# Kernel tuning notes

Measured on AMD Instinct MI355X. Metric: run time of the kernel, lower is better.

The kernel has to match this reference:

```python
import jax, jax.numpy as jnp
import numpy as np

LRELU_SLOPE = 0.2
ACT_GAIN = float(np.sqrt(2.0))  # def_gain of lrelu in StyleGAN2
CLAMP = 256.0


def _affine(w, W, b):
    # StyleGAN2 FullyConnectedLayer: runtime weight gain 1/sqrt(in_features)
    return w @ W.T * (1.0 / np.sqrt(W.shape[1])) + b[None, :]


def _gather(x, fn, pad):
    # zero rows for padding faces appended at the end, then neighborhood gather
    padded = jnp.concatenate([x, jnp.zeros((pad, x.shape[1]), x.dtype)], axis=0)
    return padded[fn]  # [N, K, C]


def _mod_texture_conv(g, styles, wc, wsd, wcr):
    # g: [N, 9, I] gathered neighborhoods; styles: [B, I]
    B, I = styles.shape
    N = g.shape[0]
    F = N // B
    # position-typed 1x1 weights: [self, 4 sides, 4 corners] -> [O, I, 9]
    W = jnp.concatenate([wc[:, :, None],
                         jnp.repeat(wsd[:, :, None], 4, axis=2),
                         jnp.repeat(wcr[:, :, None], 4, axis=2)], axis=2)
    wmod = W[None] * styles[:, None, :, None]                    # [B,O,I,9] modulate
    d = jax.lax.rsqrt(jnp.sum(wmod * wmod, axis=(2, 3)) + 1e-8)  # [B,O] demodulate
    wmod = wmod * d[:, :, None, None]
    out = jnp.einsum('bfki,boik->bfok', g.reshape(B, F, 9, I), wmod)
    return out.max(axis=3).reshape(N, -1)  # MaxPool2d((1,9)) aggregation


def _smooth_upsample(x, pool_map, fn, pad):
    # replicate coarse face features to fine faces, then smooth over 9-neighborhood
    return _gather(x[pool_map], fn, pad).mean(axis=1)


def _act(x, bias):
    # clamp_gain(lrelu(x+b), act_gain*gain, 256*gain) with gain=1
    return jnp.clip(jax.nn.leaky_relu(x + bias[None, :], LRELU_SLOPE) * ACT_GAIN, -CLAMP, CLAMP)


def setup_inputs() -> dict:
    key = jax.random.key(0)
    ks = iter(jax.random.split(key, 40))
    B, Fc, Ff = 1, 32768, 131072
    IN, OUT, GEO, COL, WD = 128, 128, 32, 3, 512
    OC1 = OUT - GEO  # 96
    PAD0, PAD1 = 1024, 4096
    nk = lambda *s: jax.random.normal(next(ks), s, jnp.float32)
    ri = lambda shape, hi: jax.random.randint(next(ks), shape, 0, hi, jnp.int32).astype(jnp.int64)
    return dict(
        x=nk(B * Fc, IN - GEO), shape_feat=nk(B * Fc, GEO), img=nk(B * Fc, COL),
        ws=nk(B, 3, WD),
        fn0=ri((B * Fc, 9), B * Fc + PAD0), fn1=ri((B * Ff, 9), B * Ff + PAD1),
        pool_map0=ri((B * Ff,), B * Fc),
        pad0=PAD0, pad1=PAD1,
        affine0_w=nk(IN, WD), affine0_b=jnp.ones((IN,), jnp.float32),
        w_center0=nk(OUT, IN), w_side0=nk(OUT, IN), w_corner0=nk(OUT, IN),
        noise_strength0=nk(1) * 0.1, bias0=nk(OUT) * 0.1, noise_const0=nk(Ff),
        affine1_w=nk(OUT, WD), affine1_b=jnp.ones((OUT,), jnp.float32),
        w_center1=nk(OC1, OUT), w_side1=nk(OC1, OUT), w_corner1=nk(OC1, OUT),
        noise_strength1=nk(1) * 0.1, bias1=nk(OC1) * 0.1, noise_const1=nk(Ff),
        affine2_w=nk(OC1, WD), affine2_b=jnp.ones((OC1,), jnp.float32),
        w_rgb=nk(COL, OC1), bias_rgb=nk(COL) * 0.1,
    )


def reference(x, shape_feat, img, ws, fn0, fn1, pool_map0, pad0, pad1,
              affine0_w, affine0_b, w_center0, w_side0, w_corner0,
              noise_strength0, bias0, noise_const0,
              affine1_w, affine1_b, w_center1, w_side1, w_corner1,
              noise_strength1, bias1, noise_const1,
              affine2_w, affine2_b, w_rgb, bias_rgb):
    B = ws.shape[0]
    h = jnp.concatenate([x, shape_feat], axis=1)  # [B*Fc, IN]
    # ---- conv0: coarse-level modulated face conv, then SmoothUpsample to fine ----
    s0 = _affine(ws[:, 0], affine0_w, affine0_b)
    h = _mod_texture_conv(_gather(h, fn0, pad0), s0, w_center0, w_side0, w_corner0)
    h = _smooth_upsample(h, pool_map0, fn1, pad1)  # [B*Ff, OUT]
    h = h + jnp.tile(noise_const0[None, :], (B, 1)).reshape(-1, 1) * noise_strength0
    h = _act(h, bias0)
    # ---- conv1: fine-level modulated face conv ----
    s1 = _affine(ws[:, 1], affine1_w, affine1_b)
    h = _mod_texture_conv(_gather(h, fn1, pad1), s1, w_center1, w_side1, w_corner1)
    h = h + jnp.tile(noise_const1[None, :], (B, 1)).reshape(-1, 1) * noise_strength1
    h = _act(h, bias1)  # [B*Ff, 96]
    # ---- torgb: 1x1 modulated conv (demodulate=False), weight_gain on styles ----
    s2 = _affine(ws[:, 2], affine2_w, affine2_b) * (1.0 / np.sqrt(w_rgb.shape[1]))
    xg = _gather(h, fn1[:, :1], pad1)[:, 0]  # kernel_size^2 == 1 -> self gather
    y = jnp.einsum('bfi,oi,bi->bfo', xg.reshape(B, -1, xg.shape[1]), w_rgb, s2)
    y = jnp.clip(y.reshape(xg.shape[0], -1) + bias_rgb[None, :], -CLAMP, CLAMP)
    img_out = _smooth_upsample(img, pool_map0, fn1, pad1) + y
    return h, img_out
```

## Files before the change

### kernel.cpp

```cpp
#include <hip/hip_runtime.h>

#define FC 32768
#define FF 131072
#define LRELU_SLOPE 0.2f
#define ACT_GAIN 1.4142135623730951f
#define CLAMP_V 256.0f

typedef __bf16 bf16x8 __attribute__((ext_vector_type(8)));
typedef float f32x4 __attribute__((ext_vector_type(4)));
typedef float f32x2 __attribute__((ext_vector_type(2)));
typedef unsigned u32x4 __attribute__((ext_vector_type(4)));
typedef unsigned u32x2 __attribute__((ext_vector_type(2)));
typedef unsigned short u16x4 __attribute__((ext_vector_type(4)));

static __device__ __forceinline__ unsigned short f2bf(float f) {
    unsigned u = __float_as_uint(f);
    u += 0x7FFFu + ((u >> 16) & 1u);
    return (unsigned short)(u >> 16);
}
static __device__ __forceinline__ unsigned packbf(float a, float b) {
    return (unsigned)f2bf(a) | ((unsigned)f2bf(b) << 16);
}
static __device__ __forceinline__ float bf2f(unsigned short u) {
    return __uint_as_float(((unsigned)u) << 16);
}
static __device__ __forceinline__ float actf(float v) {
    v = (v < 0.f) ? v * LRELU_SLOPE : v;
    v *= ACT_GAIN;
    return fminf(fmaxf(v, -CLAMP_V), CLAMP_V);
}

__global__ void k_prep2(const float* __restrict__ wsvec,
                        const float* __restrict__ a0w, const float* __restrict__ a0b,
                        const float* __restrict__ a1w, const float* __restrict__ a1b,
                        const float* __restrict__ a2w, const float* __restrict__ a2b,
                        float* __restrict__ s0, float* __restrict__ s1, float* __restrict__ s2,
                        unsigned* __restrict__ zrow)
{
    int lane = threadIdx.x & 63;
    int t = blockIdx.x * 4 + (threadIdx.x >> 6);
    if (t >= 352) {
        if (t == 352) zrow[lane] = 0u;
        return;
    }
    int level, o;
    const float *W, *bptr; float* out;
    if (t < 128)       { level = 0; o = t;       W = a0w; bptr = a0b; out = s0; }
    else if (t < 256)  { level = 1; o = t - 128; W = a1w; bptr = a1b; out = s1; }
    else               { level = 2; o = t - 256; W = a2w; bptr = a2b; out = s2; }
    const float* wrow = wsvec + level * 512;
    const float* Wr = W + (size_t)o * 512;
    f32x4 wa = *(const f32x4*)(wrow + lane * 8);
    f32x4 wb = *(const f32x4*)(wrow + lane * 8 + 4);
    f32x4 va = *(const f32x4*)(Wr + lane * 8);
    f32x4 vb = *(const f32x4*)(Wr + lane * 8 + 4);
    float acc = wa.x * va.x + wa.y * va.y + wa.z * va.z + wa.w * va.w
              + wb.x * vb.x + wb.y * vb.y + wb.z * vb.z + wb.w * vb.w;
    #pragma unroll
    for (int off = 32; off; off >>= 1) acc += __shfl_down(acc, off, 64);
    if (lane == 0) {
        float v = acc * 0.04419417382415922f + bptr[o];
        if (level == 2) v *= 0.10206207261596577f;
        out[o] = v;
    }
}

__global__ void k_misc(const float* __restrict__ x, const float* __restrict__ sf,
                       u16x4* __restrict__ xcat,
                       const int* __restrict__ fn1, const int* __restrict__ pmap,
                       int* __restrict__ cidx)
{
    int b = blockIdx.x;
    if (b < FC * 32 / 256) {
        int gid = b * 256 + threadIdx.x;
        int f = gid >> 5;
        int c4 = (gid & 31) * 4;
        f32x4 v;
        if (c4 < 96) v = *(const f32x4*)(x + (size_t)f * 96 + c4);
        else         v = *(const f32x4*)(sf + (size_t)f * 32 + (c4 - 96));
        u16x4 o;
        o.x = f2bf(v.x); o.y = f2bf(v.y); o.z = f2bf(v.z); o.w = f2bf(v.w);
        xcat[gid] = o;
    } else {
        int gid = (b - FC * 32 / 256) * 256 + threadIdx.x;
        int g = fn1[gid];
        cidx[gid] = ((unsigned)g < FF) ? pmap[g] : -1;
    }
}

__global__ void k_wmod(const float* __restrict__ wc0, const float* __restrict__ wsd0,
                       const float* __restrict__ wcr0, const float* __restrict__ s0,
                       unsigned short* __restrict__ wm0,
                       const float* __restrict__ wc1, const float* __restrict__ wsd1,
                       const float* __restrict__ wcr1, const float* __restrict__ s1,
                       unsigned short* __restrict__ wm1,
                       const float* __restrict__ wrgb, const float* __restrict__ s2,
                       float* __restrict__ wrgbmod)
{
    int b = blockIdx.x;
    int i = threadIdx.x;
    if (b == 224) {
        for (int t = i; t < 288; t += 128) {
            int c = t / 96, k = t % 96;
            wrgbmod[c * 96 + k] = wrgb[c * 96 + k] * s2[k];
        }
        return;
    }
    const float *wc, *wsd, *wcr, *s; unsigned short* out; int o, O;
    if (b < 128) { wc = wc0; wsd = wsd0; wcr = wcr0; s = s0; out = wm0; o = b; O = 128; }
    else         { wc = wc1; wsd = wsd1; wcr = wcr1; s = s1; out = wm1; o = b - 128; O = 96; }
    float sv = s[i];
    float pc = wc[o * 128 + i] * sv;
    float ps = wsd[o * 128 + i] * sv;
    float pr = wcr[o * 128 + i] * sv;
    float part = pc * pc + 4.f * ps * ps + 4.f * pr * pr;
    __shared__ float red[2];
    #pragma unroll
    for (int off = 32; off; off >>= 1) part += __shfl_down(part, off, 64);
    if ((threadIdx.x & 63) == 0) red[threadIdx.x >> 6] = part;
    __syncthreads();
    float d = rsqrtf(red[0] + red[1] + 1e-8f);
    out[(0 * O + o) * 128 + i] = f2bf(pc * d);
    out[(1 * O + o) * 128 + i] = f2bf(ps * d);
    out[(2 * O + o) * 128 + i] = f2bf(pr * d);
}

__launch_bounds__(256, 3)
__global__ void k_gemm0(const unsigned short* __restrict__ xcat, const unsigned short* __restrict__ wm,
                        unsigned* __restrict__ y0)
{
    int lane = threadIdx.x & 63;
    int w = threadIdx.x >> 6;
    int bx = blockIdx.x;
    int t = bx % 3, chunk = bx / 3;
    int fbase = (chunk * 4 + w) * 32;
    int quad = lane >> 4, l15 = lane & 15;
    const char* hb = (const char*)xcat;
    const char* wb = (const char*)wm;

    bf16x8 bfr[2][4];
    #pragma unroll
    for (int nt = 0; nt < 2; ++nt)
        #pragma unroll
        for (int s = 0; s < 4; ++s)
            bfr[nt][s] = *(const bf16x8*)(hb + (size_t)(fbase + nt * 16 + l15) * 256 + s * 64 + quad * 16);

    f32x4 acc[2][8];
    #pragma unroll
    for (int nt = 0; nt < 2; ++nt)
        #pragma unroll
        for (int mt = 0; mt < 8; ++mt)
            #pragma unroll
            for (int r = 0; r < 4; ++r) acc[nt][mt][r] = 0.f;

    #pragma unroll
    for (int s = 0; s < 4; ++s) {
        bf16x8 afr[8];
        #pragma unroll
        for (int mt = 0; mt < 8; ++mt)
            afr[mt] = *(const bf16x8*)(wb + (size_t)(((t * 128 + mt * 16 + l15) * 128 + s * 32 + quad * 8) * 2));
        #pragma unroll
        for (int nt = 0; nt < 2; ++nt)
            #pragma unroll
            for (int mt = 0; mt < 8; ++mt)
                acc[nt][mt] = __builtin_amdgcn_mfma_f32_16x16x32_bf16(afr[mt], bfr[nt][s], acc[nt][mt], 0, 0, 0);
    }

    unsigned* yt = y0 + (size_t)t * FC * 64;
    #pragma unroll
    for (int nt = 0; nt < 2; ++nt) {
        int face = fbase + nt * 16 + l15;
        #pragma unroll
        for (int mt = 0; mt < 8; ++mt) {
            u32x2 v;
            v.x = packbf(acc[nt][mt][0], acc[nt][mt][1]);
            v.y = packbf(acc[nt][mt][2], acc[nt][mt][3]);
            *(u32x2*)(yt + (size_t)face * 64 + mt * 8 + quad * 2) = v;
        }
    }
}

__global__ void k_gather0(const unsigned* __restrict__ y0, const int* __restrict__ fn0,
                          const unsigned* __restrict__ zrow, unsigned* __restrict__ hc0)
{
    int gid = blockIdx.x * 256 + threadIdx.x;
    int g = gid >> 4;
    int c = gid & 15;
    int id[9];
    #pragma unroll
    for (int j = 0; j < 9; ++j) id[j] = fn0[g * 9 + j];
    u32x4 v[9];
    #pragma unroll
    for (int j = 0; j < 9; ++j) {
        int t = (j == 0) ? 0 : (j < 5 ? 1 : 2);
        const unsigned* p = ((unsigned)id[j] < FC) ? (y0 + (size_t)t * FC * 64 + (size_t)id[j] * 64) : zrow;
        v[j] = *(const u32x4*)(p + c * 4);
    }
    u32x4 out;
    #pragma unroll
    for (int k = 0; k < 4; ++k) {
        float m0 = bf2f((unsigned short)v[0][k]);
        float m1 = bf2f((unsigned short)(v[0][k] >> 16));
        #pragma unroll
        for (int j = 1; j < 9; ++j) {
            m0 = fmaxf(m0, bf2f((unsigned short)v[j][k]));
            m1 = fmaxf(m1, bf2f((unsigned short)(v[j][k] >> 16)));
        }
        out[k] = packbf(m0, m1);
    }
    *(u32x4*)(hc0 + (size_t)g * 64 + c * 4) = out;
}

__global__ void k_upsample(const unsigned* __restrict__ hc, const int* __restrict__ cidx,
                           const float* __restrict__ nco0,
                           const float* __restrict__ ns0p, const float* __restrict__ bias0,
                           unsigned* __restrict__ h1u, const unsigned* __restrict__ zrow)
{
    int gid = blockIdx.x * 256 + threadIdx.x;
    int f = gid >> 4;
    int c = gid & 15;
    int id[9];
    #pragma unroll
    for (int j = 0; j < 9; ++j) id[j] = cidx[f * 9 + j];
    u32x4 v[9];
    #pragma unroll
    for (int j = 0; j < 9; ++j) {
        const unsigned* p = (id[j] >= 0) ? (hc + (size_t)id[j] * 64) : zrow;
        v[j] = *(const u32x4*)(p + c * 4);
    }
    float nz = nco0[f] * ns0p[0];
    f32x4 b0 = *(const f32x4*)(bias0 + c * 8);
    f32x4 b1 = *(const f32x4*)(bias0 + c * 8 + 4);
    const float inv9 = 1.f / 9.f;
    u32x4 out;
    #pragma unroll
    for (int k = 0; k < 4; ++k) {
        float a0 = 0.f, a1 = 0.f;
        #pragma unroll
        for (int j = 0; j < 9; ++j) {
            a0 += bf2f((unsigned short)v[j][k]);
            a1 += bf2f((unsigned short)(v[j][k] >> 16));
        }
        float bb0 = (k < 2) ? ((k == 0) ? b0.x : b0.z) : ((k == 2) ? b1.x : b1.z);
        float bb1 = (k < 2) ? ((k == 0) ? b0.y : b0.w) : ((k == 2) ? b1.y : b1.w);
        a0 = actf(a0 * inv9 + nz + bb0);
        a1 = actf(a1 * inv9 + nz + bb1);
        out[k] = packbf(a0, a1);
    }
    *(u32x4*)(h1u + (size_t)f * 64 + c * 4) = out;
}

__launch_bounds__(256, 4)
__global__ void k_gemm1(const unsigned short* __restrict__ h1, const unsigned short* __restrict__ wm,
                        unsigned* __restrict__ ybase)
{
    int lane = threadIdx.x & 63;
    int w = threadIdx.x >> 6;
    int bx = blockIdx.x;
    int t = bx % 3, chunk = bx / 3;
    int fbase = (chunk * 4 + w) * 32;
    int quad = lane >> 4, l15 = lane & 15;
    const char* hb = (const char*)h1;
    const char* wb = (const char*)wm;

    bf16x8 bfr[2][4];
    #pragma unroll
    for (int nt = 0; nt < 2; ++nt)
        #pragma unroll
        for (int s = 0; s < 4; ++s)
            bfr[nt][s] = *(const bf16x8*)(hb + (size_t)(fbase + nt * 16 + l15) * 256 + s * 64 + quad * 16);

    f32x4 acc[2][6];
    #pragma unroll
    for (int nt = 0; nt < 2; ++nt)
        #pragma unroll
        for (int mt = 0; mt < 6; ++mt)
            #pragma unroll
            for (int r = 0; r < 4; ++r) acc[nt][mt][r] = 0.f;

    #pragma unroll
    for (int s = 0; s < 4; ++s) {
        bf16x8 afr[6];
        #pragma unroll
        for (int mt = 0; mt < 6; ++mt)
            afr[mt] = *(const bf16x8*)(wb + (size_t)(((t * 96 + mt * 16 + l15) * 128 + s * 32 + quad * 8) * 2));
        #pragma unroll
        for (int nt = 0; nt < 2; ++nt)
            #pragma unroll
            for (int mt = 0; mt < 6; ++mt)
                acc[nt][mt] = __builtin_amdgcn_mfma_f32_16x16x32_bf16(afr[mt], bfr[nt][s], acc[nt][mt], 0, 0, 0);
    }

    unsigned* yt = ybase + (size_t)t * FF * 48;
    #pragma unroll
    for (int nt = 0; nt < 2; ++nt) {
        int face = fbase + nt * 16 + l15;
        #pragma unroll
        for (int mt = 0; mt < 6; ++mt) {
            u32x2 v;
            v.x = packbf(acc[nt][mt][0], acc[nt][mt][1]);
            v.y = packbf(acc[nt][mt][2], acc[nt][mt][3]);
            *(u32x2*)(yt + (size_t)face * 48 + mt * 8 + quad * 2) = v;
        }
    }
}

__global__ void k_gather1(const char* __restrict__ yb, const int* __restrict__ fn1,
                          const unsigned* __restrict__ zrow,
                          const float* __restrict__ nco1, const float* __restrict__ ns1p,
                          const float* __restrict__ bias1, const float* __restrict__ wrgbmod,
                          float* __restrict__ hout, f32x4* __restrict__ rgb3)
{
    int gid = blockIdx.x * 256 + threadIdx.x;
    int f = gid >> 4;
    int c = gid & 15;
    int ce = (c < 12) ? c : 11;
    int id[9];
    #pragma unroll
    for (int j = 0; j < 9; ++j) id[j] = fn1[f * 9 + j];
    u32x4 v[9];
    #pragma unroll
    for (int j = 0; j < 9; ++j) {
        int t = (j == 0) ? 0 : (j < 5 ? 1 : 2);
        const char* p = ((unsigned)id[j] < FF) ? (yb + (size_t)t * FF * 192 + (size_t)id[j] * 192) : (const char*)zrow;
        v[j] = *(const u32x4*)(p + ce * 16);
    }
    float nz = nco1[f] * ns1p[0];
    f32x4 o0, o1;
    #pragma unroll
    for (int k = 0; k < 4; ++k) {
        float m0 = bf2f((unsigned short)v[0][k]);
        float m1 = bf2f((unsigned short)(v[0][k] >> 16));
        #pragma unroll
        for (int j = 1; j < 9; ++j) {
            m0 = fmaxf(m0, bf2f((unsigned short)v[j][k]));
            m1 = fmaxf(m1, bf2f((unsigned short)(v[j][k] >> 16)));
        }
        float r0 = actf(m0 + nz + bias1[ce * 8 + k * 2]);
        float r1 = actf(m1 + nz + bias1[ce * 8 + k * 2 + 1]);
        if (k < 2) { o0[k * 2] = r0; o0[k * 2 + 1] = r1; }
        else       { o1[(k - 2) * 2] = r0; o1[(k - 2) * 2 + 1] = r1; }
    }
    float msk = (c < 12) ? 1.f : 0.f;
    f32x4 w00 = *(const f32x4*)(wrgbmod + ce * 8);
    f32x4 w01 = *(const f32x4*)(wrgbmod + ce * 8 + 4);
    f32x4 w10 = *(const f32x4*)(wrgbmod + 96 + ce * 8);
    f32x4 w11 = *(const f32x4*)(wrgbmod + 96 + ce * 8 + 4);
    f32x4 w20 = *(const f32x4*)(wrgbmod + 192 + ce * 8);
    f32x4 w21 = *(const f32x4*)(wrgbmod + 192 + ce * 8 + 4);
    float p0 = msk * (o0.x * w00.x + o0.y * w00.y + o0.z * w00.z + o0.w * w00.w
                    + o1.x * w01.x + o1.y * w01.y + o1.z * w01.z + o1.w * w01.w);
    float p1 = msk * (o0.x * w10.x + o0.y * w10.y + o0.z * w10.z + o0.w * w10.w
                    + o1.x * w11.x + o1.y * w11.y + o1.z * w11.z + o1.w * w11.w);
    float p2 = msk * (o0.x * w20.x + o0.y * w20.y + o0.z * w20.z + o0.w * w20.w
                    + o1.x * w21.x + o1.y * w21.y + o1.z * w21.z + o1.w * w21.w);
    #pragma unroll
    for (int off = 8; off; off >>= 1) {
        p0 += __shfl_xor(p0, off, 16);
        p1 += __shfl_xor(p1, off, 16);
        p2 += __shfl_xor(p2, off, 16);
    }
    if (c < 12) {
        float* op = hout + (size_t)f * 96 + c * 8;
        *(f32x4*)op = o0;
        *(f32x4*)(op + 4) = o1;
    }
    if (c == 12) {
        f32x4 o; o.x = p0; o.y = p1; o.z = p2; o.w = 0.f;
        rgb3[f] = o;
    }
}

__global__ void k_torgb2(const f32x4* __restrict__ rgb3, const int* __restrict__ fn1,
                         const int* __restrict__ cidx, const float* __restrict__ img,
                         const float* __restrict__ brgb, float* __restrict__ imgout)
{
    int f = blockIdx.x * 256 + threadIdx.x;
    int g0 = fn1[(size_t)f * 9];
    float y0 = 0.f, y1 = 0.f, y2 = 0.f;
    if ((unsigned)g0 < FF) {
        f32x4 y = rgb3[g0];
        y0 = y.x; y1 = y.y; y2 = y.z;
    }
    y0 = fminf(fmaxf(y0 + brgb[0], -CLAMP_V), CLAMP_V);
    y1 = fminf(fmaxf(y1 + brgb[1], -CLAMP_V), CLAMP_V);
    y2 = fminf(fmaxf(y2 + brgb[2], -CLAMP_V), CLAMP_V);
    float i0 = 0.f, i1 = 0.f, i2 = 0.f;
    #pragma unroll
    for (int j = 0; j < 9; ++j) {
        int id = cidx[f * 9 + j];
        if (id >= 0) {
            const float* ir = img + (size_t)id * 3;
            i0 += ir[0]; i1 += ir[1]; i2 += ir[2];
        }
    }
    const float inv9 = 1.f / 9.f;
    imgout[(size_t)f * 3 + 0] = i0 * inv9 + y0;
    imgout[(size_t)f * 3 + 1] = i1 * inv9 + y1;
    imgout[(size_t)f * 3 + 2] = i2 * inv9 + y2;
}

extern "C" void kernel_launch(void* const* d_in, const int* in_sizes, int n_in,
                              void* d_out, int out_size, void* d_ws, size_t ws_size,
                              hipStream_t stream) {
    const float* x     = (const float*)d_in[0];
    const float* sfeat = (const float*)d_in[1];
    const float* img   = (const float*)d_in[2];
    const float* wsv   = (const float*)d_in[3];
    const int* fn0     = (const int*)d_in[4];
    const int* fn1     = (const int*)d_in[5];
    const int* pmap    = (const int*)d_in[6];
    const float* a0w   = (const float*)d_in[9];
    const float* a0b   = (const float*)d_in[10];
    const float* wc0   = (const float*)d_in[11];
    const float* wsd0  = (const float*)d_in[12];
    const float* wcr0  = (const float*)d_in[13];
    const float* ns0   = (const float*)d_in[14];
    const float* bias0 = (const float*)d_in[15];
    const float* nco0  = (const float*)d_in[16];
    const float* a1w   = (const float*)d_in[17];
    const float* a1b   = (const float*)d_in[18];
    const float* wc1   = (const float*)d_in[19];
    const float* wsd1  = (const float*)d_in[20];
    const float* wcr1  = (const float*)d_in[21];
    const float* ns1   = (const float*)d_in[22];
    const float* bias1 = (const float*)d_in[23];
    const float* nco1  = (const float*)d_in[24];
    const float* a2w   = (const float*)d_in[25];
    const float* a2b   = (const float*)d_in[26];
    const float* wrgb  = (const float*)d_in[27];
    const float* brgb  = (const float*)d_in[28];

    char* wsb = (char*)d_ws;
    float* s0            = (float*)(wsb + 0);
    float* s1            = (float*)(wsb + 512);
    float* s2            = (float*)(wsb + 1024);
    float* wrgbmod       = (float*)(wsb + 1536);
    unsigned* zrow       = (unsigned*)(wsb + 4096);
    unsigned short* wm0  = (unsigned short*)(wsb + 8192);
    unsigned short* wm1  = (unsigned short*)(wsb + 8192 + 98304);
    unsigned short* xcat = (unsigned short*)(wsb + 262144);
    unsigned* y0         = (unsigned*)(wsb + 8650752);
    unsigned* hc0        = (unsigned*)(wsb + 33816576);
    unsigned short* h1   = (unsigned short*)(wsb + 42205184);
    int* cidx            = (int*)(wsb + 75759616);
    unsigned* ybase      = (unsigned*)(wsb + 80478208);
    f32x4* rgb3          = (f32x4*)(wsb + 155975680);

    float* out_h   = (float*)d_out;
    float* out_img = out_h + (size_t)FF * 96;

    k_misc<<<FC * 32 / 256 + FF * 9 / 256, 256, 0, stream>>>(x, sfeat, (u16x4*)xcat, fn1, pmap, cidx);
    k_prep2<<<89, 256, 0, stream>>>(wsv, a0w, a0b, a1w, a1b, a2w, a2b, s0, s1, s2, zrow);
    k_wmod<<<225, 128, 0, stream>>>(wc0, wsd0, wcr0, s0, wm0,
                                    wc1, wsd1, wcr1, s1, wm1, wrgb, s2, wrgbmod);
    k_gemm0<<<768, 256, 0, stream>>>(xcat, wm0, y0);
    k_gather0<<<FC * 16 / 256, 256, 0, stream>>>(y0, fn0, zrow, hc0);
    k_upsample<<<FF * 16 / 256, 256, 0, stream>>>(hc0, cidx, nco0, ns0, bias0, (unsigned*)h1, zrow);
    k_gemm1<<<3072, 256, 0, stream>>>(h1, wm1, ybase);
    k_gather1<<<FF * 16 / 256, 256, 0, stream>>>((const char*)ybase, fn1, zrow, nco1, ns1, bias1,
                                                 wrgbmod, out_h, rgb3);
    k_torgb2<<<FF / 256, 256, 0, stream>>>(rgb3, fn1, cidx, img, brgb, out_img);
}
```

Measured before the change: 313.8 us.

## Fuse neighbor gather into GEMMs and max-reduce in registers

Replaces the old GEMM-then-gather pair at both levels with kernels that gather each of the 9 neighbor rows straight into MFMA operands, run the position-typed GEMM per neighbor, and max-reduce in registers. This removes the large bf16 intermediate buffers (y0, ybase) and their write and read traffic, and the activation plus toRGB projection epilogue moves into the fused kernel. The cost is far more MFMA work: each face now does a full GEMM per neighbor instead of one per weight type, with more weight-fragment reloads per block. Gathered loads also become irregular.

New measurement: 326.6 us. 4.1% more time.

```diff
diff --git a/kernel.cpp b/kernel.cpp
--- a/kernel.cpp
+++ b/kernel.cpp
@@ -125,90 +125,78 @@
     out[(2 * O + o) * 128 + i] = f2bf(pr * d);
 }
 
-__launch_bounds__(256, 3)
-__global__ void k_gemm0(const unsigned short* __restrict__ xcat, const unsigned short* __restrict__ wm,
-                        unsigned* __restrict__ y0)
+__launch_bounds__(256, 2)
+__global__ void k_fgemm0(const unsigned short* __restrict__ xcat,
+                         const unsigned short* __restrict__ wm,
+                         const int* __restrict__ fn0,
+                         const unsigned* __restrict__ zrow,
+                         unsigned* __restrict__ hc0)
 {
     int lane = threadIdx.x & 63;
     int w = threadIdx.x >> 6;
-    int bx = blockIdx.x;
-    int t = bx % 3, chunk = bx / 3;
-    int fbase = (chunk * 4 + w) * 32;
+    int fgrp = w >> 1;
+    int mtb = (w & 1) * 4;
+    int fbase = (blockIdx.x * 2 + fgrp) * 32;
     int quad = lane >> 4, l15 = lane & 15;
     const char* hb = (const char*)xcat;
     const char* wb = (const char*)wm;
 
-    bf16x8 bfr[2][4];
+    f32x4 ymax[2][4];
     #pragma unroll
     for (int nt = 0; nt < 2; ++nt)
         #pragma unroll
-        for (int s = 0; s < 4; ++s)
-            bfr[nt][s] = *(const bf16x8*)(hb + (size_t)(fbase + nt * 16 + l15) * 256 + s * 64 + quad * 16);
-
-    f32x4 acc[2][8];
-    #pragma unroll
-    for (int nt = 0; nt < 2; ++nt)
-        #pragma unroll
-        for (int mt = 0; mt < 8; ++mt)
-            #pragma unroll
-            for (int r = 0; r < 4; ++r) acc[nt][mt][r] = 0.f;
-
-    #pragma unroll
-    for (int s = 0; s < 4; ++s) {
-        bf16x8 afr[8];
-        #pragma unroll
-        for (int mt = 0; mt < 8; ++mt)
-            afr[mt] = *(const bf16x8*)(wb + (size_t)(((t * 128 + mt * 16 + l15) * 128 + s * 32 + quad * 8) * 2));
+        for (int mi = 0; mi < 4; ++mi)
+            #pragma unroll
+            for (int r = 0; r < 4; ++r) ymax[nt][mi][r] = -3.0e38f;
+
+    #pragma unroll
+    for (int j = 0; j < 9; ++j) {
+        const int t = (j == 0) ? 0 : ((j < 5) ? 1 : 2);
+        bf16x8 bfr[2][4];
+        #pragma unroll
+        for (int nt = 0; nt < 2; ++nt) {
+            int idj = fn0[(size_t)(fbase + nt * 16 + l15) * 9 + j];
+            const char* src = ((unsigned)idj < FC) ? (hb + (size_t)idj * 256) : (const char*)zrow;
+            #pragma unroll
+            for (int s = 0; s < 4; ++s)
+                bfr[nt][s] = *(const bf16x8*)(src + s * 64 + quad * 16);
+        }
+        f32x4 acc[2][4];
         #pragma unroll
         for (int nt = 0; nt < 2; ++nt)
             #pragma unroll
-            for (int mt = 0; mt < 8; ++mt)
-                acc[nt][mt] = __builtin_amdgcn_mfma_f32_16x16x32_bf16(afr[mt], bfr[nt][s], acc[nt][mt], 0, 0, 0);
-    }
-
-    unsigned* yt = y0 + (size_t)t * FC * 64;
+            for (int mi = 0; mi < 4; ++mi)
+                #pragma unroll
+                for (int r = 0; r < 4; ++r) acc[nt][mi][r] = 0.f;
+        #pragma unroll
+        for (int s = 0; s < 4; ++s) {
+            #pragma unroll
+            for (int mi = 0; mi < 4; ++mi) {
+                bf16x8 afr = *(const bf16x8*)(wb + (size_t)(((t * 128 + (mtb + mi) * 16 + l15) * 128 + s * 32 + quad * 8) * 2));
+                acc[0][mi] = __builtin_amdgcn_mfma_f32_16x16x32_bf16(afr, bfr[0][s], acc[0][mi], 0, 0, 0);
+                acc[1][mi] = __builtin_amdgcn_mfma_f32_16x16x32_bf16(afr, bfr[1][s], acc[1][mi], 0, 0, 0);
+            }
+        }
+        #pragma unroll
+        for (int nt = 0; nt < 2; ++nt)
+            #pragma unroll
+            for (int mi = 0; mi < 4; ++mi)
+                #pragma unroll
+                for (int r = 0; r < 4; ++r)
+                    ymax[nt][mi][r] = fmaxf(ymax[nt][mi][r], acc[nt][mi][r]);
+    }
+
     #pragma unroll
     for (int nt = 0; nt < 2; ++nt) {
         int face = fbase + nt * 16 + l15;
         #pragma unroll
-        for (int mt = 0; mt < 8; ++mt) {
+        for (int mi = 0; mi < 4; ++mi) {
             u32x2 v;
-            v.x = packbf(acc[nt][mt][0], acc[nt][mt][1]);
-            v.y = packbf(acc[nt][mt][2], acc[nt][mt][3]);
-            *(u32x2*)(yt + (size_t)face * 64 + mt * 8 + quad * 2) = v;
-        }
-    }
-}
-
-__global__ void k_gather0(const unsigned* __restrict__ y0, const int* __restrict__ fn0,
-                          const unsigned* __restrict__ zrow, unsigned* __restrict__ hc0)
-{
-    int gid = blockIdx.x * 256 + threadIdx.x;
-    int g = gid >> 4;
-    int c = gid & 15;
-    int id[9];
-    #pragma unroll
-    for (int j = 0; j < 9; ++j) id[j] = fn0[g * 9 + j];
-    u32x4 v[9];
-    #pragma unroll
-    for (int j = 0; j < 9; ++j) {
-        int t = (j == 0) ? 0 : (j < 5 ? 1 : 2);
-        const unsigned* p = ((unsigned)id[j] < FC) ? (y0 + (size_t)t * FC * 64 + (size_t)id[j] * 64) : zrow;
-        v[j] = *(const u32x4*)(p + c * 4);
-    }
-    u32x4 out;
-    #pragma unroll
-    for (int k = 0; k < 4; ++k) {
-        float m0 = bf2f((unsigned short)v[0][k]);
-        float m1 = bf2f((unsigned short)(v[0][k] >> 16));
-        #pragma unroll
-        for (int j = 1; j < 9; ++j) {
-            m0 = fmaxf(m0, bf2f((unsigned short)v[j][k]));
-            m1 = fmaxf(m1, bf2f((unsigned short)(v[j][k] >> 16)));
-        }
-        out[k] = packbf(m0, m1);
-    }
-    *(u32x4*)(hc0 + (size_t)g * 64 + c * 4) = out;
+            v.x = packbf(ymax[nt][mi][0], ymax[nt][mi][1]);
+            v.y = packbf(ymax[nt][mi][2], ymax[nt][mi][3]);
+            *(u32x2*)(hc0 + (size_t)face * 64 + (mtb + mi) * 8 + quad * 2) = v;
+        }
+    }
 }
 
 __global__ void k_upsample(const unsigned* __restrict__ hc, const int* __restrict__ cidx,
@@ -250,124 +238,94 @@
     *(u32x4*)(h1u + (size_t)f * 64 + c * 4) = out;
 }
 
-__launch_bounds__(256, 4)
-__global__ void k_gemm1(const unsigned short* __restrict__ h1, const unsigned short* __restrict__ wm,
-                        unsigned* __restrict__ ybase)
+__launch_bounds__(256, 2)
+__global__ void k_fgemm1(const unsigned short* __restrict__ h1,
+                         const unsigned short* __restrict__ wm,
+                         const int* __restrict__ fn1,
+                         const unsigned* __restrict__ zrow,
+                         const float* __restrict__ nco1, const float* __restrict__ ns1p,
+                         const float* __restrict__ bias1, const float* __restrict__ wrgbmod,
+                         float* __restrict__ hout, f32x4* __restrict__ rgb3)
 {
     int lane = threadIdx.x & 63;
     int w = threadIdx.x >> 6;
-    int bx = blockIdx.x;
-    int t = bx % 3, chunk = bx / 3;
-    int fbase = (chunk * 4 + w) * 32;
+    int fbase = (blockIdx.x * 4 + w) * 32;
     int quad = lane >> 4, l15 = lane & 15;
     const char* hb = (const char*)h1;
     const char* wb = (const char*)wm;
 
-    bf16x8 bfr[2][4];
+    f32x4 ymax[2][6];
     #pragma unroll
     for (int nt = 0; nt < 2; ++nt)
         #pragma unroll
-        for (int s = 0; s < 4; ++s)
-            bfr[nt][s] = *(const bf16x8*)(hb + (size_t)(fbase + nt * 16 + l15) * 256 + s * 64 + quad * 16);
-
-    f32x4 acc[2][6];
-    #pragma unroll
-    for (int nt = 0; nt < 2; ++nt)
-        #pragma unroll
         for (int mt = 0; mt < 6; ++mt)
             #pragma unroll
-            for (int r = 0; r < 4; ++r) acc[nt][mt][r] = 0.f;
-
-    #pragma unroll
-    for (int s = 0; s < 4; ++s) {
-        bf16x8 afr[6];
-        #pragma unroll
-        for (int mt = 0; mt < 6; ++mt)
-            afr[mt] = *(const bf16x8*)(wb + (size_t)(((t * 96 + mt * 16 + l15) * 128 + s * 32 + quad * 8) * 2));
+            for (int r = 0; r < 4; ++r) ymax[nt][mt][r] = -3.0e38f;
+
+    #pragma unroll
+    for (int j = 0; j < 9; ++j) {
+        const int t = (j == 0) ? 0 : ((j < 5) ? 1 : 2);
+        bf16x8 bfr[2][4];
+        #pragma unroll
+        for (int nt = 0; nt < 2; ++nt) {
+            int idj = fn1[(size_t)(fbase + nt * 16 + l15) * 9 + j];
+            const char* src = ((unsigned)idj < FF) ? (hb + (size_t)idj * 256) : (const char*)zrow;
+            #pragma unroll
+            for (int s = 0; s < 4; ++s)
+                bfr[nt][s] = *(const bf16x8*)(src + s * 64 + quad * 16);
+        }
+        f32x4 acc[2][6];
         #pragma unroll
         for (int nt = 0; nt < 2; ++nt)
             #pragma unroll
             for (int mt = 0; mt < 6; ++mt)
-                acc[nt][mt] = __builtin_amdgcn_mfma_f32_16x16x32_bf16(afr[mt], bfr[nt][s], acc[nt][mt], 0, 0, 0);
-    }
-
-    unsigned* yt = ybase + (size_t)t * FF * 48;
+                #pragma unroll
+                for (int r = 0; r < 4; ++r) acc[nt][mt][r] = 0.f;
+        #pragma unroll
+        for (int s = 0; s < 4; ++s) {
+            #pragma unroll
+            for (int mt = 0; mt < 6; ++mt) {
+                bf16x8 afr = *(const bf16x8*)(wb + (size_t)(((t * 96 + mt * 16 + l15) * 128 + s * 32 + quad * 8) * 2));
+                acc[0][mt] = __builtin_amdgcn_mfma_f32_16x16x32_bf16(afr, bfr[0][s], acc[0][mt], 0, 0, 0);
+                acc[1][mt] = __builtin_amdgcn_mfma_f32_16x16x32_bf16(afr, bfr[1][s], acc[1][mt], 0, 0, 0);
+            }
+        }
+        #pragma unroll
+        for (int nt = 0; nt < 2; ++nt)
+            #pragma unroll
+            for (int mt = 0; mt < 6; ++mt)
+                #pragma unroll
+                for (int r = 0; r < 4; ++r)
+                    ymax[nt][mt][r] = fmaxf(ymax[nt][mt][r], acc[nt][mt][r]);
+    }
+
+    float ns1 = ns1p[0];
     #pragma unroll
     for (int nt = 0; nt < 2; ++nt) {
         int face = fbase + nt * 16 + l15;
+        float nz = nco1[face] * ns1;
+        float p0 = 0.f, p1 = 0.f, p2 = 0.f;
         #pragma unroll
         for (int mt = 0; mt < 6; ++mt) {
-            u32x2 v;
-            v.x = packbf(acc[nt][mt][0], acc[nt][mt][1]);
-            v.y = packbf(acc[nt][mt][2], acc[nt][mt][3]);
-            *(u32x2*)(yt + (size_t)face * 48 + mt * 8 + quad * 2) = v;
-        }
-    }
-}
-
-__global__ void k_gather1(const char* __restrict__ yb, const int* __restrict__ fn1,
-                          const unsigned* __restrict__ zrow,
-                          const float* __restrict__ nco1, const float* __restrict__ ns1p,
-                          const float* __restrict__ bias1, const float* __restrict__ wrgbmod,
-                          float* __restrict__ hout, f32x4* __restrict__ rgb3)
-{
-    int gid = blockIdx.x * 256 + threadIdx.x;
-    int f = gid >> 4;
-    int c = gid & 15;
-    int ce = (c < 12) ? c : 11;
-    int id[9];
-    #pragma unroll
-    for (int j = 0; j < 9; ++j) id[j] = fn1[f * 9 + j];
-    u32x4 v[9];
-    #pragma unroll
-    for (int j = 0; j < 9; ++j) {
-        int t = (j == 0) ? 0 : (j < 5 ? 1 : 2);
-        const char* p = ((unsigned)id[j] < FF) ? (yb + (size_t)t * FF * 192 + (size_t)id[j] * 192) : (const char*)zrow;
-        v[j] = *(const u32x4*)(p + ce * 16);
-    }
-    float nz = nco1[f] * ns1p[0];
-    f32x4 o0, o1;
-    #pragma unroll
-    for (int k = 0; k < 4; ++k) {
-        float m0 = bf2f((unsigned short)v[0][k]);
-        float m1 = bf2f((unsigned short)(v[0][k] >> 16));
-        #pragma unroll
-        for (int j = 1; j < 9; ++j) {
-            m0 = fmaxf(m0, bf2f((unsigned short)v[j][k]));
-            m1 = fmaxf(m1, bf2f((unsigned short)(v[j][k] >> 16)));
-        }
-        float r0 = actf(m0 + nz + bias1[ce * 8 + k * 2]);
-        float r1 = actf(m1 + nz + bias1[ce * 8 + k * 2 + 1]);
-        if (k < 2) { o0[k * 2] = r0; o0[k * 2 + 1] = r1; }
-        else       { o1[(k - 2) * 2] = r0; o1[(k - 2) * 2 + 1] = r1; }
-    }
-    float msk = (c < 12) ? 1.f : 0.f;
-    f32x4 w00 = *(const f32x4*)(wrgbmod + ce * 8);
-    f32x4 w01 = *(const f32x4*)(wrgbmod + ce * 8 + 4);
-    f32x4 w10 = *(const f32x4*)(wrgbmod + 96 + ce * 8);
-    f32x4 w11 = *(const f32x4*)(wrgbmod + 96 + ce * 8 + 4);
-    f32x4 w20 = *(const f32x4*)(wrgbmod + 192 + ce * 8);
-    f32x4 w21 = *(const f32x4*)(wrgbmod + 192 + ce * 8 + 4);
-    float p0 = msk * (o0.x * w00.x + o0.y * w00.y + o0.z * w00.z + o0.w * w00.w
-                    + o1.x * w01.x + o1.y * w01.y + o1.z * w01.z + o1.w * w01.w);
-    float p1 = msk * (o0.x * w10.x + o0.y * w10.y + o0.z * w10.z + o0.w * w10.w
-                    + o1.x * w11.x + o1.y * w11.y + o1.z * w11.z + o1.w * w11.w);
-    float p2 = msk * (o0.x * w20.x + o0.y * w20.y + o0.z * w20.z + o0.w * w20.w
-                    + o1.x * w21.x + o1.y * w21.y + o1.z * w21.z + o1.w * w21.w);
-    #pragma unroll
-    for (int off = 8; off; off >>= 1) {
-        p0 += __shfl_xor(p0, off, 16);
-        p1 += __shfl_xor(p1, off, 16);
-        p2 += __shfl_xor(p2, off, 16);
-    }
-    if (c < 12) {
-        float* op = hout + (size_t)f * 96 + c * 8;
-        *(f32x4*)op = o0;
-        *(f32x4*)(op + 4) = o1;
-    }
-    if (c == 12) {
-        f32x4 o; o.x = p0; o.y = p1; o.z = p2; o.w = 0.f;
-        rgb3[f] = o;
+            f32x4 bv = *(const f32x4*)(bias1 + mt * 16 + quad * 4);
+            f32x4 hv;
+            #pragma unroll
+            for (int r = 0; r < 4; ++r) hv[r] = actf(ymax[nt][mt][r] + nz + bv[r]);
+            *(f32x4*)(hout + (size_t)face * 96 + mt * 16 + quad * 4) = hv;
+            f32x4 w0 = *(const f32x4*)(wrgbmod + mt * 16 + quad * 4);
+            f32x4 w1 = *(const f32x4*)(wrgbmod + 96 + mt * 16 + quad * 4);
+            f32x4 w2 = *(const f32x4*)(wrgbmod + 192 + mt * 16 + quad * 4);
+            p0 += hv.x * w0.x + hv.y * w0.y + hv.z * w0.z + hv.w * w0.w;
+            p1 += hv.x * w1.x + hv.y * w1.y + hv.z * w1.z + hv.w * w1.w;
+            p2 += hv.x * w2.x + hv.y * w2.y + hv.z * w2.z + hv.w * w2.w;
+        }
+        p0 += __shfl_xor(p0, 16, 64); p0 += __shfl_xor(p0, 32, 64);
+        p1 += __shfl_xor(p1, 16, 64); p1 += __shfl_xor(p1, 32, 64);
+        p2 += __shfl_xor(p2, 16, 64); p2 += __shfl_xor(p2, 32, 64);
+        if (quad == 0) {
+            f32x4 o; o.x = p0; o.y = p1; o.z = p2; o.w = 0.f;
+            rgb3[face] = o;
+        }
     }
 }
 
@@ -440,11 +398,9 @@
     unsigned short* wm0  = (unsigned short*)(wsb + 8192);
     unsigned short* wm1  = (unsigned short*)(wsb + 8192 + 98304);
     unsigned short* xcat = (unsigned short*)(wsb + 262144);
-    unsigned* y0         = (unsigned*)(wsb + 8650752);
     unsigned* hc0        = (unsigned*)(wsb + 33816576);
     unsigned short* h1   = (unsigned short*)(wsb + 42205184);
     int* cidx            = (int*)(wsb + 75759616);
-    unsigned* ybase      = (unsigned*)(wsb + 80478208);
     f32x4* rgb3          = (f32x4*)(wsb + 155975680);
 
     float* out_h   = (float*)d_out;
@@ -454,11 +410,9 @@
     k_prep2<<<89, 256, 0, stream>>>(wsv, a0w, a0b, a1w, a1b, a2w, a2b, s0, s1, s2, zrow);
     k_wmod<<<225, 128, 0, stream>>>(wc0, wsd0, wcr0, s0, wm0,
                                     wc1, wsd1, wcr1, s1, wm1, wrgb, s2, wrgbmod);
-    k_gemm0<<<768, 256, 0, stream>>>(xcat, wm0, y0);
-    k_gather0<<<FC * 16 / 256, 256, 0, stream>>>(y0, fn0, zrow, hc0);
+    k_fgemm0<<<FC / 64, 256, 0, stream>>>(xcat, wm0, fn0, zrow, hc0);
     k_upsample<<<FF * 16 / 256, 256, 0, stream>>>(hc0, cidx, nco0, ns0, bias0, (unsigned*)h1, zrow);
-    k_gemm1<<<3072, 256, 0, stream>>>(h1, wm1, ybase);
-    k_gather1<<<FF * 16 / 256, 256, 0, stream>>>((const char*)ybase, fn1, zrow, nco1, ns1, bias1,
-                                                 wrgbmod, out_h, rgb3);
+    k_fgemm1<<<FF / 128, 256, 0, stream>>>(h1, wm1, fn1, zrow, nco1, ns1, bias1, wrgbmod,
+                                           out_h, rgb3);
     k_torgb2<<<FF / 256, 256, 0, stream>>>(rgb3, fn1, cidx, img, brgb, out_img);
 }
```
